# Performance work log

Measured on AMD Instinct MI355X. Metric: run time of the kernel, lower is better.

## Reference

```python
import jax, jax.numpy as jnp
import numpy as np

N = 100000
IN_DIM = 256
HID = 128
E = 1600000


def setup_inputs() -> dict:
    key = jax.random.key(0)
    ks = jax.random.split(key, 6)
    x = jax.random.normal(ks[0], (N, IN_DIM), dtype=jnp.float32)
    edge_index = jax.random.randint(ks[1], (2, E), 0, N, dtype=jnp.int64)
    # GCNConv weight (hidden, in) and bias (hidden); decoder Linear (in, hidden) + bias
    s_in = 1.0 / np.sqrt(IN_DIM)
    s_h = 1.0 / np.sqrt(HID)
    W_enc = jax.random.uniform(ks[2], (HID, IN_DIM), jnp.float32, -s_in, s_in)
    b_enc = jnp.zeros((HID,), jnp.float32)
    W_dec = jax.random.uniform(ks[3], (IN_DIM, HID), jnp.float32, -s_h, s_h)
    b_dec = jax.random.uniform(ks[4], (IN_DIM,), jnp.float32, -s_h, s_h)
    return {"x": x, "edge_index": edge_index, "W_enc": W_enc, "b_enc": b_enc,
            "W_dec": W_dec, "b_dec": b_dec}


def gcn_conv(x, edge_index, W, b):
    # Linear transform first (PyG GCNConv): h = x @ W^T  -> [N, HID]
    h = x @ W.T
    # Add self-loops
    loops = jnp.arange(N, dtype=edge_index.dtype)
    row = jnp.concatenate([edge_index[0], loops])  # source
    col = jnp.concatenate([edge_index[1], loops])  # target
    # Symmetric normalization: deg over targets (incl. self-loops)
    deg = jax.ops.segment_sum(jnp.ones_like(col, dtype=h.dtype), col, num_segments=N)
    dinv = jax.lax.rsqrt(deg)  # deg >= 1 due to self-loops
    norm = dinv[row] * dinv[col]  # [E+N]
    msg = h[row] * norm[:, None]  # gather + scale  [E+N, HID]
    agg = jax.ops.segment_sum(msg, col, num_segments=N)  # scatter-add
    return agg + b


def reference(x, edge_index, W_enc, b_enc, W_dec, b_dec):
    z = jax.nn.relu(gcn_conv(x, edge_index, W_enc, b_enc))
    x_recon = z @ W_dec.T + b_dec
    return (z, x_recon)
```

## Files before the change

### kernel.cpp

```cpp
#include <hip/hip_runtime.h>
#include <hip/hip_bf16.h>

#define NDIM 256
#define HDIM 128
#define NPAD 100352
#define LDS1_STRIDE 264
#define LDS2_STRIDE 136
#define P2CAP 6144

typedef __bf16 bf16_t;
typedef bf16_t bf16x2 __attribute__((ext_vector_type(2)));
typedef bf16_t bf16x4 __attribute__((ext_vector_type(4)));
typedef bf16_t bf16x8 __attribute__((ext_vector_type(8)));
typedef float f32x2 __attribute__((ext_vector_type(2)));
typedef float f32x4 __attribute__((ext_vector_type(4)));

__global__ __launch_bounds__(256) void k_prep(const float* __restrict__ We, bf16_t* __restrict__ wpe,
                                              const float* __restrict__ Wd, bf16_t* __restrict__ wpd) {
    const int b = blockIdx.x, t = threadIdx.x;
    const bool enc = b < 16;
    const int i = (enc ? b : b - 16) * 256 + t;
    const int lane = i & 63;
    const int fr = lane & 15, kg = lane >> 4;
    int nf, kk32, K, NF;
    const float* W;
    bf16_t* wp;
    if (enc) { nf = (i >> 6) & 7;  kk32 = i >> 9;  K = NDIM; NF = 8;  W = We; wp = wpe; }
    else     { nf = (i >> 6) & 15; kk32 = i >> 10; K = HDIM; NF = 16; W = Wd; wp = wpd; }
    const float* src = &W[(size_t)(nf * 16 + fr) * K + kk32 * 32 + kg * 8];
    const f32x4 a0 = *reinterpret_cast<const f32x4*>(src);
    const f32x4 a1 = *reinterpret_cast<const f32x4*>(src + 4);
    bf16x8 o;
    o[0] = (bf16_t)a0[0]; o[1] = (bf16_t)a0[1]; o[2] = (bf16_t)a0[2]; o[3] = (bf16_t)a0[3];
    o[4] = (bf16_t)a1[0]; o[5] = (bf16_t)a1[1]; o[6] = (bf16_t)a1[2]; o[7] = (bf16_t)a1[3];
    reinterpret_cast<bf16x8*>(wp)[(kk32 * NF + nf) * 64 + lane] = o;
}

template<int K, int NC, bool OUT_BF16>
__device__ __forceinline__ void mfma_epi(const bf16x8* af,
                                         const bf16_t* __restrict__ Wp,
                                         const float* __restrict__ bias,
                                         void* __restrict__ Cout,
                                         const int bid, const int nrows) {
    const int lane = threadIdx.x & 63;
    const int wv = threadIdx.x >> 6;
    const int fr = lane & 15;
    const int kg = lane >> 4;
    constexpr int NF = NC / 16, NK = K / 32;

    const bf16x8* wp = reinterpret_cast<const bf16x8*>(Wp);
    f32x4 acc[NF];
    const f32x4 zero4 = {0.f, 0.f, 0.f, 0.f};
    #pragma unroll
    for (int nf = 0; nf < NF; ++nf) acc[nf] = zero4;

    #pragma unroll
    for (int k = 0; k < NK; ++k) {
        #pragma unroll
        for (int nf = 0; nf < NF; ++nf)
            acc[nf] = __builtin_amdgcn_mfma_f32_16x16x32_bf16(af[k], wp[(k * NF + nf) * 64 + lane], acc[nf], 0, 0, 0);
    }

    const long long rbase = (long long)bid * 64 + wv * 16 + kg * 4;
    #pragma unroll
    for (int nf = 0; nf < NF; ++nf) {
        const int c = nf * 16 + fr;
        const float bv = bias ? bias[c] : 0.f;
        #pragma unroll
        for (int i = 0; i < 4; ++i) {
            const long long r = rbase + i;
            if (r < nrows) {
                const float v = acc[nf][i] + bv;
                if (OUT_BF16) ((bf16_t*)Cout)[r * NC + c] = (bf16_t)v;
                else          __builtin_nontemporal_store(v, &((float*)Cout)[r * NC + c]);
            }
        }
    }
}

__device__ __forceinline__ void gemm1_body(const int bid, const float* __restrict__ x,
                                           const bf16_t* __restrict__ wpe,
                                           bf16_t* __restrict__ hb, const int nrows,
                                           bf16_t* lds) {
    const int t = threadIdx.x;
    const long long rowbase = (long long)bid * 64;
    #pragma unroll
    for (int p = 0; p < 16; ++p) {
        const int s = p * 256 + t;
        const int r = s >> 6, c4 = s & 63;
        long long gr = rowbase + r;
        if (gr >= nrows) gr = nrows - 1;
        const f32x4 v = __builtin_nontemporal_load(reinterpret_cast<const f32x4*>(&x[gr * NDIM + c4 * 4]));
        bf16x4 o;
        o[0] = (bf16_t)v[0]; o[1] = (bf16_t)v[1]; o[2] = (bf16_t)v[2]; o[3] = (bf16_t)v[3];
        *reinterpret_cast<bf16x4*>(&lds[r * LDS1_STRIDE + c4 * 4]) = o;
    }
    __syncthreads();
    const int lane = t & 63, wv = t >> 6, fr = lane & 15, kg = lane >> 4;
    bf16x8 af[8];
    #pragma unroll
    for (int k = 0; k < 8; ++k)
        af[k] = *reinterpret_cast<const bf16x8*>(&lds[(wv * 16 + fr) * LDS1_STRIDE + k * 32 + kg * 8]);
    mfma_epi<NDIM, HDIM, true>(af, wpe, nullptr, hb, bid, nrows);
}

__device__ __forceinline__ void p1a_body(const int blk, const int* __restrict__ col,
                                         int* __restrict__ bcnt, const int E_,
                                         const int nbkt, const int epb, int* lhist) {
    const int t = threadIdx.x;
    for (int i = t; i < nbkt; i += 256) lhist[i] = 0;
    __syncthreads();
    const int base = blk * epb;
    const int cnt = min(E_ - base, epb);
    for (int i = t; i < cnt; i += 256)
        atomicAdd(&lhist[col[base + i] >> 8], 1);
    __syncthreads();
    for (int i = t; i < nbkt; i += 256)
        bcnt[i * 256 + blk] = lhist[i];
}

__global__ __launch_bounds__(256) void k_fused(const float* __restrict__ x,
                                               const bf16_t* __restrict__ wpe,
                                               bf16_t* __restrict__ hb, const int nrows,
                                               const int* __restrict__ col,
                                               int* __restrict__ bcnt,
                                               const int E_, const int nbkt, const int epb,
                                               const int G1) {
    __shared__ __align__(16) bf16_t lds[64 * LDS1_STRIDE];
    const int b = blockIdx.x;
    if (b < G1) gemm1_body(b, x, wpe, hb, nrows, lds);
    else        p1a_body(b - G1, col, bcnt, E_, nbkt, epb, (int*)lds);
}

__global__ __launch_bounds__(256) void k_scanB1(const int* __restrict__ bcnt,
                                                int* __restrict__ bsum, const int M) {
    __shared__ int s[256];
    const int b = blockIdx.x, t = threadIdx.x;
    const int i0 = b * 1024 + t * 4;
    int4 v = make_int4(0, 0, 0, 0);
    if (i0 + 4 <= M) v = *reinterpret_cast<const int4*>(&bcnt[i0]);
    else if (i0 < M) {
        const int k = M - i0;
        v.x = bcnt[i0];
        if (k > 1) v.y = bcnt[i0 + 1];
        if (k > 2) v.z = bcnt[i0 + 2];
    }
    s[t] = v.x + v.y + v.z + v.w;
    __syncthreads();
    for (int d = 128; d > 0; d >>= 1) {
        if (t < d) s[t] += s[t + d];
        __syncthreads();
    }
    if (t == 0) bsum[b] = s[0];
}

__global__ __launch_bounds__(128) void k_scanB2(const int* __restrict__ bsum,
                                                int* __restrict__ bofs,
                                                int* __restrict__ bbase,
                                                const int nb, const int M) {
    __shared__ int s[128];
    const int t = threadIdx.x;
    const int v = (t < nb) ? bsum[t] : 0;
    s[t] = v;
    __syncthreads();
    for (int d = 1; d < 128; d <<= 1) {
        int xx = (t >= d) ? s[t - d] : 0;
        __syncthreads();
        s[t] += xx;
        __syncthreads();
    }
    if (t < nb) bofs[t] = s[t] - v;
    if (t == nb - 1) bbase[M] = s[t];
}

__global__ __launch_bounds__(256) void k_scanB3(const int* __restrict__ bcnt,
                                                const int* __restrict__ bofs,
                                                int* __restrict__ bbase, const int M) {
    __shared__ int s[256];
    const int b = blockIdx.x, t = threadIdx.x;
    const int i0 = b * 1024 + t * 4;
    int4 v = make_int4(0, 0, 0, 0);
    if (i0 + 4 <= M) v = *reinterpret_cast<const int4*>(&bcnt[i0]);
    else if (i0 < M) {
        const int k = M - i0;
        v.x = bcnt[i0];
        if (k > 1) v.y = bcnt[i0 + 1];
        if (k > 2) v.z = bcnt[i0 + 2];
    }
    const int tsum = v.x + v.y + v.z + v.w;
    s[t] = tsum;
    __syncthreads();
    for (int d = 1; d < 256; d <<= 1) {
        int xx = (t >= d) ? s[t - d] : 0;
        __syncthreads();
        s[t] += xx;
        __syncthreads();
    }
    const int excl = s[t] - tsum + bofs[b];
    int4 o;
    o.x = excl; o.y = excl + v.x; o.z = o.y + v.y; o.w = o.z + v.z;
    if (i0 + 4 <= M) *reinterpret_cast<int4*>(&bbase[i0]) = o;
    else if (i0 < M) {
        const int k = M - i0;
        bbase[i0] = o.x;
        if (k > 1) bbase[i0 + 1] = o.y;
        if (k > 2) bbase[i0 + 2] = o.z;
    }
}

__global__ __launch_bounds__(256) void k_p1b(const int* __restrict__ row,
                                             const int* __restrict__ col,
                                             const int* __restrict__ bbase,
                                             int* __restrict__ pbuf,
                                             const int E_, const int nbkt, const int epb) {
    __shared__ int lcur[512];
    const int blk = blockIdx.x, t = threadIdx.x;
    for (int i = t; i < nbkt; i += 256) lcur[i] = bbase[i * 256 + blk];
    __syncthreads();
    const int base = blk * epb;
    const int cnt = min(E_ - base, epb);
    for (int i = t; i < cnt; i += 256) {
        const int c = col[base + i];
        const int r = row[base + i];
        const int pos = atomicAdd(&lcur[c >> 8], 1);
        pbuf[pos] = r | ((c & 255) << 17);
    }
}

__global__ __launch_bounds__(256) void k_p2(const int* __restrict__ pbuf,
                                            const int* __restrict__ bbase,
                                            int* __restrict__ ebuf,
                                            int* __restrict__ goff, int* __restrict__ gcnt,
                                            float* __restrict__ dinv,
                                            const int n, const int E_) {
    __shared__ int lcnt[256], lscan[256], lcur[256];
    __shared__ __align__(16) int ecache[P2CAP];
    const int b = blockIdx.x, t = threadIdx.x;
    const int start = bbase[b * 256];
    const int end = bbase[(b + 1) * 256];
    const int size = end - start;
    const bool inlds = size <= P2CAP;
    lcnt[t] = 0; lcur[t] = 0;
    __syncthreads();
    if (inlds) {
        for (int i = t; i < size; i += 256) {
            const int e = pbuf[start + i];
            ecache[i] = e;
            atomicAdd(&lcnt[(e >> 17) & 255], 1);
        }
    } else {
        for (int i = t; i < size; i += 256)
            atomicAdd(&lcnt[(pbuf[start + i] >> 17) & 255], 1);
    }
    __syncthreads();
    const int v = lcnt[t];
    lscan[t] = v;
    __syncthreads();
    for (int d = 1; d < 256; d <<= 1) {
        int xx = (t >= d) ? lscan[t - d] : 0;
        __syncthreads();
        lscan[t] += xx;
        __syncthreads();
    }
    const int excl = lscan[t] - v;
    const int node = (b << 8) + t;
    if (node < n) {
        goff[node] = start + excl;
        gcnt[node] = v;
        dinv[node] = rsqrtf((float)(v + 1));
    }
    lscan[t] = excl;
    __syncthreads();
    for (int i = t; i < size; i += 256) {
        const int e = inlds ? ecache[i] : pbuf[start + i];
        const int li = (e >> 17) & 255;
        const int rk = atomicAdd(&lcur[li], 1);
        ebuf[start + lscan[li] + rk] = e & 0x1FFFF;
    }
}

__device__ __forceinline__ float bflo(unsigned u) { return __uint_as_float(u << 16); }
__device__ __forceinline__ float bfhi(unsigned u) { return __uint_as_float(u & 0xffff0000u); }

__global__ __launch_bounds__(256) void k_agg(const int* __restrict__ ebuf,
                                             const int* __restrict__ off,
                                             const int* __restrict__ cnt,
                                             const float* __restrict__ dinv,
                                             const unsigned* __restrict__ hb,
                                             const float* __restrict__ benc,
                                             float* __restrict__ z,
                                             bf16_t* __restrict__ zb, int n) {
    const int node = blockIdx.x * 4 + (threadIdx.x >> 6);
    const int lane = threadIdx.x & 63;
    if (node >= n) return;
    const float dc = dinv[node];
    const unsigned hself = hb[(size_t)node * 64 + lane];
    float acc0 = bflo(hself) * (dc * dc);
    float acc1 = bfhi(hself) * (dc * dc);
    const int base = off[node], m = cnt[node];
    int j = 0;
    for (; j + 16 <= m; j += 16) {
        int r[16]; float d[16]; unsigned u[16];
        #pragma unroll
        for (int q = 0; q < 16; ++q) r[q] = __builtin_nontemporal_load(&ebuf[base + j + q]);
        #pragma unroll
        for (int q = 0; q < 16; ++q) u[q] = hb[(size_t)r[q] * 64 + lane];
        #pragma unroll
        for (int q = 0; q < 16; ++q) d[q] = dinv[r[q]];
        #pragma unroll
        for (int q = 0; q < 16; ++q) {
            const float nq = d[q] * dc;
            acc0 += bflo(u[q]) * nq;
            acc1 += bfhi(u[q]) * nq;
        }
    }
    for (; j + 4 <= m; j += 4) {
        int r[4]; float d[4]; unsigned u[4];
        #pragma unroll
        for (int q = 0; q < 4; ++q) r[q] = __builtin_nontemporal_load(&ebuf[base + j + q]);
        #pragma unroll
        for (int q = 0; q < 4; ++q) u[q] = hb[(size_t)r[q] * 64 + lane];
        #pragma unroll
        for (int q = 0; q < 4; ++q) d[q] = dinv[r[q]];
        #pragma unroll
        for (int q = 0; q < 4; ++q) {
            const float nq = d[q] * dc;
            acc0 += bflo(u[q]) * nq;
            acc1 += bfhi(u[q]) * nq;
        }
    }
    for (; j < m; ++j) {
        const int r = __builtin_nontemporal_load(&ebuf[base + j]);
        const float nr = dinv[r] * dc;
        const unsigned u = hb[(size_t)r * 64 + lane];
        acc0 += bflo(u) * nr;
        acc1 += bfhi(u) * nr;
    }
    f32x2 o;
    o[0] = fmaxf(acc0 + benc[lane * 2], 0.f);
    o[1] = fmaxf(acc1 + benc[lane * 2 + 1], 0.f);
    __builtin_nontemporal_store(o, reinterpret_cast<f32x2*>(&z[(size_t)node * HDIM + lane * 2]));
    bf16x2 ob;
    ob[0] = (bf16_t)o[0];
    ob[1] = (bf16_t)o[1];
    __builtin_nontemporal_store(__builtin_bit_cast(unsigned, ob),
                                reinterpret_cast<unsigned*>(&zb[(size_t)node * HDIM + lane * 2]));
}

__global__ __launch_bounds__(256) void k_gemm2(const bf16_t* __restrict__ zb,
                                               const bf16_t* __restrict__ wpd,
                                               const float* __restrict__ bias,
                                               float* __restrict__ xrec, const int nrows) {
    __shared__ __align__(16) bf16_t lds[64 * LDS2_STRIDE];
    const int t = threadIdx.x;
    const long long rowbase = (long long)blockIdx.x * 64;
    #pragma unroll
    for (int p = 0; p < 4; ++p) {
        const int s = p * 256 + t;
        const int r = s >> 4, c8 = s & 15;
        long long gr = rowbase + r;
        if (gr >= nrows) gr = nrows - 1;
        const bf16x8 v = *reinterpret_cast<const bf16x8*>(&zb[gr * HDIM + c8 * 8]);
        *reinterpret_cast<bf16x8*>(&lds[r * LDS2_STRIDE + c8 * 8]) = v;
    }
    __syncthreads();
    const int lane = t & 63, wv = t >> 6, fr = lane & 15, kg = lane >> 4;
    bf16x8 af[4];
    #pragma unroll
    for (int k = 0; k < 4; ++k)
        af[k] = *reinterpret_cast<const bf16x8*>(&lds[(wv * 16 + fr) * LDS2_STRIDE + k * 32 + kg * 8]);
    mfma_epi<HDIM, NDIM, false>(af, wpd, bias, xrec, blockIdx.x, nrows);
}

extern "C" void kernel_launch(void* const* d_in, const int* in_sizes, int n_in,
                              void* d_out, int out_size, void* d_ws, size_t ws_size,
                              hipStream_t stream) {
    const float* x     = (const float*)d_in[0];
    const int*   ei    = (const int*)d_in[1];
    const float* W_enc = (const float*)d_in[2];
    const float* b_enc = (const float*)d_in[3];
    const float* W_dec = (const float*)d_in[4];
    const float* b_dec = (const float*)d_in[5];

    const int N = in_sizes[0] / NDIM;
    const int E = in_sizes[1] / 2;
    const int* row = ei;
    const int* col = ei + E;

    const int NBKT = (N + 255) >> 8;
    const int M = NBKT * 256;
    const int EPB = (E + 255) / 256;
    const int G1 = (N + 63) / 64;
    const int SB = (M + 1023) / 1024;

    char* wsp = (char*)d_ws;
    int*    pbuf = (int*)wsp;
    bf16_t* zb   = (bf16_t*)wsp;
    const size_t r0 = ((size_t)N * HDIM * 2 > (size_t)E * 4) ? (size_t)N * HDIM * 2 : (size_t)E * 4;
    bf16_t* hb   = (bf16_t*)(wsp + r0);
    int*    ebuf = (int*)(wsp + r0 + (size_t)N * HDIM * 2);
    int*    goff = ebuf + E;
    int*    gcnt = goff + NPAD;
    float*  dinv = (float*)(gcnt + NPAD);
    int*    bcnt = (int*)(dinv + NPAD);
    int*    bbase = bcnt + M;
    int*    bsum = bbase + M + 1;
    int*    bofs = bsum + 128;
    bf16_t* wpe  = (bf16_t*)(bofs + 128);
    bf16_t* wpd  = wpe + HDIM * NDIM;

    float* z    = (float*)d_out;
    float* xrec = (float*)d_out + (size_t)N * HDIM;

    k_prep<<<32, 256, 0, stream>>>(W_enc, wpe, W_dec, wpd);

    k_fused<<<G1 + 256, 256, 0, stream>>>(x, wpe, hb, N, col, bcnt, E, NBKT, EPB, G1);

    k_scanB1<<<SB, 256, 0, stream>>>(bcnt, bsum, M);
    k_scanB2<<<1, 128, 0, stream>>>(bsum, bofs, bbase, SB, M);
    k_scanB3<<<SB, 256, 0, stream>>>(bcnt, bofs, bbase, M);

    k_p1b<<<256, 256, 0, stream>>>(row, col, bbase, pbuf, E, NBKT, EPB);

    k_p2<<<NBKT, 256, 0, stream>>>(pbuf, bbase, ebuf, goff, gcnt, dinv, N, E);

    k_agg<<<(N + 3) / 4, 256, 0, stream>>>(ebuf, goff, gcnt, dinv, (const unsigned*)hb, b_enc, z, zb, N);

    k_gemm2<<<G1, 256, 0, stream>>>(zb, wpd, b_dec, xrec, N);
}
```

Measured before the change: 242.6 us.

## Pre-scale h rows by source dinv in p2, apply target dinv once

The p2 kernel now stores each node's dinv in LDS and rescales that node's bf16 row of h by its own dinv in place. The aggregation kernel can then drop the per-edge dinv gather and multiply, summing pre-scaled rows and applying the target dinv once with the bias. This removes a random 4-byte gather and an FMA per edge in the hot gather loop. In exchange, p2 does an extra read-modify-write pass over h, and there is one more bf16 rounding step. Nontemporal hints on the ebuf loads and the z/zb stores are also dropped.

```diff
diff --git a/kernel.cpp b/kernel.cpp
--- a/kernel.cpp
+++ b/kernel.cpp
@@ -14,6 +14,9 @@
 typedef bf16_t bf16x8 __attribute__((ext_vector_type(8)));
 typedef float f32x2 __attribute__((ext_vector_type(2)));
 typedef float f32x4 __attribute__((ext_vector_type(4)));
+
+__device__ __forceinline__ float bflo(unsigned u) { return __uint_as_float(u << 16); }
+__device__ __forceinline__ float bfhi(unsigned u) { return __uint_as_float(u & 0xffff0000u); }
 
 __global__ __launch_bounds__(256) void k_prep(const float* __restrict__ We, bf16_t* __restrict__ wpe,
                                               const float* __restrict__ Wd, bf16_t* __restrict__ wpd) {
@@ -232,8 +235,10 @@
                                             int* __restrict__ ebuf,
                                             int* __restrict__ goff, int* __restrict__ gcnt,
                                             float* __restrict__ dinv,
+                                            unsigned* __restrict__ hbw,
                                             const int n, const int E_) {
     __shared__ int lcnt[256], lscan[256], lcur[256];
+    __shared__ float ldinv[256];
     __shared__ __align__(16) int ecache[P2CAP];
     const int b = blockIdx.x, t = threadIdx.x;
     const int start = bbase[b * 256];
@@ -264,11 +269,14 @@
     }
     const int excl = lscan[t] - v;
     const int node = (b << 8) + t;
+    float dvv = 0.f;
     if (node < n) {
+        dvv = rsqrtf((float)(v + 1));
         goff[node] = start + excl;
         gcnt[node] = v;
-        dinv[node] = rsqrtf((float)(v + 1));
-    }
+        dinv[node] = dvv;
+    }
+    ldinv[t] = dvv;
     lscan[t] = excl;
     __syncthreads();
     for (int i = t; i < size; i += 256) {
@@ -277,10 +285,20 @@
         const int rk = atomicAdd(&lcur[li], 1);
         ebuf[start + lscan[li] + rk] = e & 0x1FFFF;
     }
-}
-
-__device__ __forceinline__ float bflo(unsigned u) { return __uint_as_float(u << 16); }
-__device__ __forceinline__ float bfhi(unsigned u) { return __uint_as_float(u & 0xffff0000u); }
+    const int wv = t >> 6, lane = t & 63;
+    #pragma unroll 4
+    for (int rr = wv * 64; rr < wv * 64 + 64; ++rr) {
+        const int nd = (b << 8) + rr;
+        if (nd >= n) break;
+        const float dv = ldinv[rr];
+        unsigned* p = &hbw[(size_t)nd * 64 + lane];
+        const unsigned u = *p;
+        bf16x2 pk;
+        pk[0] = (bf16_t)(bflo(u) * dv);
+        pk[1] = (bf16_t)(bfhi(u) * dv);
+        *p = __builtin_bit_cast(unsigned, pk);
+    }
+}
 
 __global__ __launch_bounds__(256) void k_agg(const int* __restrict__ ebuf,
                                              const int* __restrict__ off,
@@ -295,56 +313,47 @@
     if (node >= n) return;
     const float dc = dinv[node];
     const unsigned hself = hb[(size_t)node * 64 + lane];
-    float acc0 = bflo(hself) * (dc * dc);
-    float acc1 = bfhi(hself) * (dc * dc);
+    float acc0 = bflo(hself);
+    float acc1 = bfhi(hself);
     const int base = off[node], m = cnt[node];
     int j = 0;
     for (; j + 16 <= m; j += 16) {
-        int r[16]; float d[16]; unsigned u[16];
-        #pragma unroll
-        for (int q = 0; q < 16; ++q) r[q] = __builtin_nontemporal_load(&ebuf[base + j + q]);
+        int r[16]; unsigned u[16];
+        #pragma unroll
+        for (int q = 0; q < 16; ++q) r[q] = ebuf[base + j + q];
         #pragma unroll
         for (int q = 0; q < 16; ++q) u[q] = hb[(size_t)r[q] * 64 + lane];
         #pragma unroll
-        for (int q = 0; q < 16; ++q) d[q] = dinv[r[q]];
-        #pragma unroll
         for (int q = 0; q < 16; ++q) {
-            const float nq = d[q] * dc;
-            acc0 += bflo(u[q]) * nq;
-            acc1 += bfhi(u[q]) * nq;
+            acc0 += bflo(u[q]);
+            acc1 += bfhi(u[q]);
         }
     }
     for (; j + 4 <= m; j += 4) {
-        int r[4]; float d[4]; unsigned u[4];
-        #pragma unroll
-        for (int q = 0; q < 4; ++q) r[q] = __builtin_nontemporal_load(&ebuf[base + j + q]);
+        int r[4]; unsigned u[4];
+        #pragma unroll
+        for (int q = 0; q < 4; ++q) r[q] = ebuf[base + j + q];
         #pragma unroll
         for (int q = 0; q < 4; ++q) u[q] = hb[(size_t)r[q] * 64 + lane];
         #pragma unroll
-        for (int q = 0; q < 4; ++q) d[q] = dinv[r[q]];
-        #pragma unroll
         for (int q = 0; q < 4; ++q) {
-            const float nq = d[q] * dc;
-            acc0 += bflo(u[q]) * nq;
-            acc1 += bfhi(u[q]) * nq;
+            acc0 += bflo(u[q]);
+            acc1 += bfhi(u[q]);
         }
     }
     for (; j < m; ++j) {
-        const int r = __builtin_nontemporal_load(&ebuf[base + j]);
-        const float nr = dinv[r] * dc;
-        const unsigned u = hb[(size_t)r * 64 + lane];
-        acc0 += bflo(u) * nr;
-        acc1 += bfhi(u) * nr;
+        const unsigned u = hb[(size_t)ebuf[base + j] * 64 + lane];
+        acc0 += bflo(u);
+        acc1 += bfhi(u);
     }
     f32x2 o;
-    o[0] = fmaxf(acc0 + benc[lane * 2], 0.f);
-    o[1] = fmaxf(acc1 + benc[lane * 2 + 1], 0.f);
-    __builtin_nontemporal_store(o, reinterpret_cast<f32x2*>(&z[(size_t)node * HDIM + lane * 2]));
+    o[0] = fmaxf(fmaf(dc, acc0, benc[lane * 2]), 0.f);
+    o[1] = fmaxf(fmaf(dc, acc1, benc[lane * 2 + 1]), 0.f);
+    *reinterpret_cast<f32x2*>(&z[(size_t)node * HDIM + lane * 2]) = o;
     bf16x2 ob;
     ob[0] = (bf16_t)o[0];
     ob[1] = (bf16_t)o[1];
-    __builtin_nontemporal_store(__builtin_bit_cast(unsigned, ob),
-                                reinterpret_cast<unsigned*>(&zb[(size_t)node * HDIM + lane * 2]));
+    *reinterpret_cast<bf16x2*>(&zb[(size_t)node * HDIM + lane * 2]) = ob;
 }
 
 __global__ __launch_bounds__(256) void k_gemm2(const bf16_t* __restrict__ zb,
@@ -422,7 +431,7 @@
 
     k_p1b<<<256, 256, 0, stream>>>(row, col, bbase, pbuf, E, NBKT, EPB);
 
-    k_p2<<<NBKT, 256, 0, stream>>>(pbuf, bbase, ebuf, goff, gcnt, dinv, N, E);
+    k_p2<<<NBKT, 256, 0, stream>>>(pbuf, bbase, ebuf, goff, gcnt, dinv, (unsigned*)hb, N, E);
 
     k_agg<<<(N + 3) / 4, 256, 0, stream>>>(ebuf, goff, gcnt, dinv, (const unsigned*)hb, b_enc, z, zb, N);
 
```

New measurement: 224.1 us (median of 2 runs). -7.6%, faster.
